# Performance work log

Measured on AMD Instinct MI355X. Metric: run time of the kernel, lower is better.

## Reference

```python
import jax, jax.numpy as jnp
import numpy as np

DIN = 512      # input feature dim (din)
HEADS = 8
DHEAD = 64
DIM = HEADS * DHEAD  # 512
NTOT = 12288   # total nodes across all graphs
NBATCH = 32    # number of graphs
NMAX = 512     # padded max nodes per graph (<= pf_threshold ~562 -> softmax branch)
EPS = 1e-5


def setup_inputs() -> dict:
    key = jax.random.key(0)
    ks = jax.random.split(key, 7)
    z = jax.random.normal(ks[0], (NTOT, DIN), jnp.float32)
    src = jnp.sort(jax.random.randint(ks[1], (NTOT,), 0, NBATCH)).astype(jnp.int32)
    w_scale = 1.0 / np.sqrt(DIN)
    Wq = jax.random.normal(ks[2], (DIN, DIM), jnp.float32) * w_scale
    Wk = jax.random.normal(ks[3], (DIN, DIM), jnp.float32) * w_scale
    Wv = jax.random.normal(ks[4], (DIN, DIM), jnp.float32) * w_scale
    Wo = jax.random.normal(ks[5], (DIM, DIM), jnp.float32) * w_scale
    bo = jnp.zeros((DIM,), jnp.float32)
    ln_gamma = jnp.ones((DIN,), jnp.float32)
    ln_beta = jnp.zeros((DIN,), jnp.float32)
    return {"z": z, "src": src, "ln_gamma": ln_gamma, "ln_beta": ln_beta,
            "Wq": Wq, "Wk": Wk, "Wv": Wv, "Wo": Wo, "bo": bo,
            "n_max": NMAX, "n_batch": NBATCH}


def reference(z, src, ln_gamma, ln_beta, Wq, Wk, Wv, Wo, bo, n_max, n_batch):
    # --- LayerNorm(din) ---
    mu = jnp.mean(z, axis=-1, keepdims=True)
    var = jnp.mean(jnp.square(z - mu), axis=-1, keepdims=True)
    zn = (z - mu) * jax.lax.rsqrt(var + EPS) * ln_gamma + ln_beta

    # --- to_dense_batch(zn, src): src is sorted graph-id per node ---
    ntot = z.shape[0]
    counts = jnp.bincount(src, length=n_batch)                    # [B]
    starts = jnp.concatenate([jnp.zeros((1,), counts.dtype), jnp.cumsum(counts)[:-1]])
    pos = jnp.arange(ntot) - starts[src]                          # position within graph
    x = jnp.zeros((n_batch, n_max, DIN), zn.dtype).at[src, pos].set(zn)   # [B,N,din]
    mask = jnp.zeros((n_batch, n_max), bool).at[src, pos].set(True)       # [B,N]

    # --- q/k/v projections, split heads: b n (h d) -> b h n d ---
    def heads(t):
        return t.reshape(n_batch, n_max, HEADS, DHEAD).transpose(0, 2, 1, 3)
    q = heads(x @ Wq)
    k = heads(x @ Wk)
    v = heads(x @ Wv)

    # --- manual masked softmax attention (N <= pf_threshold branch) ---
    s = jnp.einsum('bhmd,bhnd->bhmn', q, k)
    s = jnp.where(mask[:, None, None, :], s, -jnp.inf)
    a = jax.nn.softmax(s * (DHEAD ** -0.5), axis=-1)
    o = jnp.einsum('bhmn,bhnd->bhmd', a, v)

    # --- merge heads, gather valid rows (out[mask]), output projection ---
    o = o.transpose(0, 2, 1, 3).reshape(n_batch, n_max, DIM)
    h = o[src, pos] @ Wo + bo                                     # [Ntot, DIM]
    return h
```

## Files before the change

kernel.cpp:

```cpp
#include <hip/hip_runtime.h>
#include <hip/hip_bf16.h>
#include <math.h>

#define DIN 512
#define DIM 512
#define NHEADS 8
#define DHEAD 64
#define NB 32
#define NPAD 512
#define NPTOT (NB * NPAD)

typedef __attribute__((ext_vector_type(8))) short bf16x8;
typedef __attribute__((ext_vector_type(8))) unsigned short u16x8;
typedef __attribute__((ext_vector_type(4))) float f32x4;

typedef __attribute__((address_space(3))) unsigned int lds_u32;
typedef __attribute__((address_space(1))) const unsigned int g_u32;

__device__ __forceinline__ void gll16(const unsigned short* g, unsigned short* l) {
  __builtin_amdgcn_global_load_lds((g_u32*)g, (lds_u32*)l, 16, 0, 0);
}

__device__ inline unsigned short f2bf(float x) {
  unsigned int u = __float_as_uint(x);
  unsigned int r = (u + 0x7FFFu + ((u >> 16) & 1u)) >> 16;
  return (unsigned short)r;
}

__global__ __launch_bounds__(256) void prep_kernel(const float* __restrict__ z,
                                                   const float* __restrict__ gamma,
                                                   const float* __restrict__ beta,
                                                   const int* __restrict__ src,
                                                   const float* __restrict__ Wq,
                                                   const float* __restrict__ Wk,
                                                   const float* __restrict__ Wv,
                                                   const float* __restrict__ Wo,
                                                   unsigned short* __restrict__ zn,
                                                   int* __restrict__ starts,
                                                   int* __restrict__ dstrow,
                                                   unsigned short* __restrict__ WtQKV,
                                                   unsigned short* __restrict__ WtO,
                                                   int ntot) {
  __shared__ float tile[32][33];
  int b = blockIdx.x;
  int nln = ntot >> 2;
  int nmap = (ntot + 255) >> 8;
  if (b < nln) {
    int wave = b * 4 + (threadIdx.x >> 6);
    int lane = threadIdx.x & 63;
    const float* row = z + (size_t)wave * DIN;
    float4 a = ((const float4*)row)[lane];
    float4 bb = ((const float4*)row)[64 + lane];
    float s  = a.x + a.y + a.z + a.w + bb.x + bb.y + bb.z + bb.w;
    float sq = a.x*a.x + a.y*a.y + a.z*a.z + a.w*a.w
             + bb.x*bb.x + bb.y*bb.y + bb.z*bb.z + bb.w*bb.w;
#pragma unroll
    for (int off = 32; off; off >>= 1) {
      s  += __shfl_xor(s, off);
      sq += __shfl_xor(sq, off);
    }
    float mu  = s * (1.0f / DIN);
    float var = sq * (1.0f / DIN) - mu * mu;
    float r   = rsqrtf(var + 1e-5f);
    float4 g0 = ((const float4*)gamma)[lane];
    float4 g1 = ((const float4*)gamma)[64 + lane];
    float4 b0 = ((const float4*)beta)[lane];
    float4 b1 = ((const float4*)beta)[64 + lane];
    ushort4 o0, o1;
    o0.x = f2bf((a.x - mu) * r * g0.x + b0.x);
    o0.y = f2bf((a.y - mu) * r * g0.y + b0.y);
    o0.z = f2bf((a.z - mu) * r * g0.z + b0.z);
    o0.w = f2bf((a.w - mu) * r * g0.w + b0.w);
    o1.x = f2bf((bb.x - mu) * r * g1.x + b1.x);
    o1.y = f2bf((bb.y - mu) * r * g1.y + b1.y);
    o1.z = f2bf((bb.z - mu) * r * g1.z + b1.z);
    o1.w = f2bf((bb.w - mu) * r * g1.w + b1.w);
    ((ushort4*)(zn + (size_t)wave * DIN))[lane] = o0;
    ((ushort4*)(zn + (size_t)wave * DIN))[64 + lane] = o1;
  } else if (b < nln + nmap) {
    int bid = b - nln;
    if (bid == 0 && threadIdx.x <= NB) {
      int gg = threadIdx.x;
      int lo = 0, hi = ntot;
      while (lo < hi) { int mid = (lo + hi) >> 1; if (src[mid] < gg) lo = mid + 1; else hi = mid; }
      starts[gg] = lo;
    }
    int i = bid * 256 + threadIdx.x;
    if (i < ntot) {
      int gg = src[i];
      int lo = 0, hi = ntot;
      while (lo < hi) { int mid = (lo + hi) >> 1; if (src[mid] < gg) lo = mid + 1; else hi = mid; }
      dstrow[i] = gg * NPAD + (i - lo);
    }
  } else {
    int idx = b - nln - nmap;
    int zz = idx >> 8;
    int rem = idx & 255;
    const float* W; unsigned short* Wt;
    if (zz == 0)      { W = Wq; Wt = WtQKV; }
    else if (zz == 1) { W = Wk; Wt = WtQKV + (size_t)512 * DIN; }
    else if (zz == 2) { W = Wv; Wt = WtQKV + (size_t)1024 * DIN; }
    else              { W = Wo; Wt = WtO; }
    int k0 = (rem & 15) * 32;
    int n0 = (rem >> 4) * 32;
    int tx = threadIdx.x & 31;
    int ty = threadIdx.x >> 5;
#pragma unroll
    for (int i = 0; i < 4; i++)
      tile[ty + i * 8][tx] = W[(size_t)(k0 + ty + i * 8) * DIM + n0 + tx];
    __syncthreads();
#pragma unroll
    for (int i = 0; i < 4; i++)
      Wt[(size_t)(n0 + ty + i * 8) * DIN + k0 + tx] = f2bf(tile[tx][ty + i * 8]);
  }
}

template <int NCOLS, bool BIAS, bool OUT_F32, bool REMAP>
__global__ __launch_bounds__(256) void gemm_staged(const unsigned short* __restrict__ A,
                                                   const unsigned short* __restrict__ Bt,
                                                   const float* __restrict__ bias,
                                                   const int* __restrict__ remap,
                                                   unsigned short* __restrict__ Cbf,
                                                   float* __restrict__ Cf) {
  __shared__ unsigned short smem[16384];
  int tid = threadIdx.x, lane = tid & 63, wv = tid >> 6;
  int col = lane & 15, quad = lane >> 4;
  int m0 = blockIdx.x * 128, n0 = blockIdx.y * 128;
  int msub = (wv & 1) * 64, nsub = (wv >> 1) * 64;

  int srow = lane >> 2;
  int cswz = (((lane & 3) ^ ((lane >> 3) & 3))) * 8;

  f32x4 acc[4][4];
#pragma unroll
  for (int i = 0; i < 4; i++)
#pragma unroll
    for (int j = 0; j < 4; j++) acc[i][j] = (f32x4){0.f, 0.f, 0.f, 0.f};

  auto stage = [&](int ks, int nb) {
    const unsigned short* Ab = A  + (size_t)m0 * DIN + ks * 32;
    const unsigned short* Bb = Bt + (size_t)n0 * DIN + ks * 32;
#pragma unroll
    for (int i = 0; i < 2; i++) {
      int t = wv * 2 + i;
      gll16(Ab + (size_t)(t * 16 + srow) * DIN + cswz, smem + nb * 4096 + t * 512);
      gll16(Bb + (size_t)(t * 16 + srow) * DIN + cswz, smem + 8192 + nb * 4096 + t * 512);
    }
  };

  stage(0, 0);
#pragma unroll 2
  for (int ks = 0; ks < 16; ks++) {
    int cur = ks & 1;
    __syncthreads();
    if (ks + 1 < 16) stage(ks + 1, 1 - cur);
    bf16x8 af[4], bfr[4];
#pragma unroll
    for (int mt = 0; mt < 4; mt++) {
      int row = msub + mt * 16 + col;
      af[mt] = *(const bf16x8*)&smem[cur * 4096 + row * 32 + ((quad ^ ((row >> 1) & 3)) * 8)];
    }
#pragma unroll
    for (int nt = 0; nt < 4; nt++) {
      int row = nsub + nt * 16 + col;
      bfr[nt] = *(const bf16x8*)&smem[8192 + cur * 4096 + row * 32 + ((quad ^ ((row >> 1) & 3)) * 8)];
    }
#pragma unroll
    for (int mt = 0; mt < 4; mt++)
#pragma unroll
      for (int nt = 0; nt < 4; nt++)
        acc[mt][nt] = __builtin_amdgcn_mfma_f32_16x16x32_bf16(af[mt], bfr[nt], acc[mt][nt], 0, 0, 0);
  }

  if (!OUT_F32) {
    __syncthreads();
#pragma unroll
    for (int mt = 0; mt < 4; mt++)
#pragma unroll
      for (int r = 0; r < 4; r++) {
        int row = msub + mt * 16 + quad * 4 + r;
#pragma unroll
        for (int nt = 0; nt < 4; nt++) {
          int c = nsub + nt * 16 + col;
          float v = acc[mt][nt][r] + (BIAS ? bias[n0 + c] : 0.f);
          smem[row * 128 + (((c >> 3) ^ (quad << 1)) * 8) + (c & 7)] = f2bf(v);
        }
      }
    __syncthreads();
#pragma unroll
    for (int pass = 0; pass < 8; pass++) {
      int row = pass * 16 + (tid >> 4);
      int sw  = ((row >> 2) & 3) << 1;
      int ch  = tid & 15;
      u16x8 vv = *(const u16x8*)&smem[row * 128 + ((ch ^ sw) * 8)];
      int drow = REMAP ? remap[m0 + row] : (m0 + row);
      *(u16x8*)(Cbf + (size_t)drow * NCOLS + n0 + ch * 8) = vv;
    }
  } else {
#pragma unroll
    for (int mt = 0; mt < 4; mt++) {
#pragma unroll
      for (int r = 0; r < 4; r++) {
        int mrow = m0 + msub + mt * 16 + quad * 4 + r;
#pragma unroll
        for (int nt = 0; nt < 4; nt++) {
          int ncol = n0 + nsub + nt * 16 + col;
          Cf[(size_t)mrow * NCOLS + ncol] = acc[mt][nt][r] + (BIAS ? bias[ncol] : 0.f);
        }
      }
    }
  }
}

__global__ __launch_bounds__(256, 3) void fattn_kernel(const unsigned short* __restrict__ qkvp,
                                                       const int* __restrict__ starts,
                                                       unsigned short* __restrict__ obuf) {
  __shared__ unsigned short Kbuf[2][64 * 64];
  __shared__ unsigned short Vbuf[2][64 * 64];
  __shared__ unsigned short Plds[4][32 * 64];
  int g = blockIdx.x, h = blockIdx.y, qt = blockIdx.z;
  int st = starts[g];
  int n  = starts[g + 1] - st;
  int q0b = qt * 128;
  if (q0b >= n) return;
  int tid = threadIdx.x, lane = tid & 63, wv = tid >> 6;
  int col = lane & 15, quad = lane >> 4;
  int q0 = q0b + wv * 32;
  bool active = q0 < n;
  int ntiles = (n + 63) >> 6;

  bf16x8 qf[2][2];
  if (active) {
#pragma unroll
    for (int a = 0; a < 2; a++) {
      const unsigned short* qp = qkvp + (size_t)(g * NPAD + q0 + a * 16 + col) * 1536 + h * 64 + quad * 8;
      qf[a][0] = *(const bf16x8*)(qp);
      qf[a][1] = *(const bf16x8*)(qp + 32);
    }
  }

  int srow = tid >> 2;
  int sc   = (tid & 3) * 2;
  int woff0 = srow * 64 + ((sc ^ (srow & 7)) * 8);
  int woff1 = srow * 64 + (((sc + 1) ^ (srow & 7)) * 8);
  u16x8 kreg0, kreg1, vreg0, vreg1;
  auto loadregs = [&](int kt) {
    const unsigned short* kp = qkvp + (size_t)(g * NPAD + kt + srow) * 1536 + 512 + h * 64 + sc * 8;
    kreg0 = *(const u16x8*)(kp);
    kreg1 = *(const u16x8*)(kp + 8);
    vreg0 = *(const u16x8*)(kp + 512);
    vreg1 = *(const u16x8*)(kp + 520);
  };
  auto writelds = [&](int bsel) {
    *(u16x8*)&Kbuf[bsel][woff0] = kreg0;
    *(u16x8*)&Kbuf[bsel][woff1] = kreg1;
#pragma unroll
    for (int i = 0; i < 8; i++) {
      int c0 = sc * 8 + i;
      int c1 = sc * 8 + 8 + i;
      Vbuf[bsel][c0 * 64 + (((srow >> 3) ^ ((c0 >> 4) << 1) ^ (c0 & 7)) * 8) + (srow & 7)] = vreg0[i];
      Vbuf[bsel][c1 * 64 + (((srow >> 3) ^ ((c1 >> 4) << 1) ^ (c1 & 7)) * 8) + (srow & 7)] = vreg1[i];
    }
  };

  bf16x8 onesv;
#pragma unroll
  for (int i = 0; i < 8; i++) onesv[i] = (short)0x3F80;

  f32x4 oa[2][4];
  f32x4 lacc[2];
#pragma unroll
  for (int a = 0; a < 2; a++) {
    lacc[a] = (f32x4){0.f, 0.f, 0.f, 0.f};
#pragma unroll
    for (int i = 0; i < 4; i++) oa[a][i] = (f32x4){0.f, 0.f, 0.f, 0.f};
  }

  loadregs(0);
  writelds(0);
  __syncthreads();

  for (int t = 0; t < ntiles; t++) {
    int cur = t & 1;
    if (t + 1 < ntiles) loadregs((t + 1) * 64);
    if (active) {
      f32x4 s[2][4];
#pragma unroll
      for (int a = 0; a < 2; a++)
#pragma unroll
        for (int j = 0; j < 4; j++) s[a][j] = (f32x4){0.f, 0.f, 0.f, 0.f};
#pragma unroll
      for (int j = 0; j < 4; j++) {
        int R = j * 16 + col;
        bf16x8 kf0 = *(const bf16x8*)&Kbuf[cur][R * 64 + ((quad ^ (R & 7)) * 8)];
        bf16x8 kf1 = *(const bf16x8*)&Kbuf[cur][R * 64 + (((4 + quad) ^ (R & 7)) * 8)];
        s[0][j] = __builtin_amdgcn_mfma_f32_16x16x32_bf16(qf[0][0], kf0, s[0][j], 0, 0, 0);
        s[0][j] = __builtin_amdgcn_mfma_f32_16x16x32_bf16(qf[0][1], kf1, s[0][j], 0, 0, 0);
        s[1][j] = __builtin_amdgcn_mfma_f32_16x16x32_bf16(qf[1][0], kf0, s[1][j], 0, 0, 0);
        s[1][j] = __builtin_amdgcn_mfma_f32_16x16x32_bf16(qf[1][1], kf1, s[1][j], 0, 0, 0);
      }
      int kt = t * 64;
#pragma unroll
      for (int j = 0; j < 4; j++) {
        bool valid = (kt + j * 16 + col) < n;
#pragma unroll
        for (int a = 0; a < 2; a++)
#pragma unroll
          for (int r = 0; r < 4; r++)
            s[a][j][r] = valid ? __expf(s[a][j][r] * 0.125f) : 0.f;
      }
#pragma unroll
      for (int a = 0; a < 2; a++)
#pragma unroll
        for (int r = 0; r < 4; r++) {
          int R = a * 16 + quad * 4 + r;
#pragma unroll
          for (int j = 0; j < 4; j++) {
            int chunk = j * 2 + (col >> 3);
            Plds[wv][R * 64 + ((chunk ^ (R & 7)) * 8) + (col & 7)] = f2bf(s[a][j][r]);
          }
        }
      __builtin_amdgcn_fence(__ATOMIC_ACQ_REL, "workgroup");
      bf16x8 pf[2][2];
#pragma unroll
      for (int a = 0; a < 2; a++) {
        int R = a * 16 + col;
        pf[a][0] = *(const bf16x8*)&Plds[wv][R * 64 + ((quad ^ (col & 7)) * 8)];
        pf[a][1] = *(const bf16x8*)&Plds[wv][R * 64 + (((4 + quad) ^ (col & 7)) * 8)];
      }
#pragma unroll
      for (int dt = 0; dt < 4; dt++) {
        int R = dt * 16 + col;
        int gR = ((R >> 4) << 1) ^ (R & 7);
        bf16x8 vf0 = *(const bf16x8*)&Vbuf[cur][R * 64 + ((quad ^ gR) * 8)];
        bf16x8 vf1 = *(const bf16x8*)&Vbuf[cur][R * 64 + (((quad + 4) ^ gR) * 8)];
        oa[0][dt] = __builtin_amdgcn_mfma_f32_16x16x32_bf16(pf[0][0], vf0, oa[0][dt], 0, 0, 0);
        oa[0][dt] = __builtin_amdgcn_mfma_f32_16x16x32_bf16(pf[0][1], vf1, oa[0][dt], 0, 0, 0);
        oa[1][dt] = __builtin_amdgcn_mfma_f32_16x16x32_bf16(pf[1][0], vf0, oa[1][dt], 0, 0, 0);
        oa[1][dt] = __builtin_amdgcn_mfma_f32_16x16x32_bf16(pf[1][1], vf1, oa[1][dt], 0, 0, 0);
      }
      lacc[0] = __builtin_amdgcn_mfma_f32_16x16x32_bf16(pf[0][0], onesv, lacc[0], 0, 0, 0);
      lacc[0] = __builtin_amdgcn_mfma_f32_16x16x32_bf16(pf[0][1], onesv, lacc[0], 0, 0, 0);
      lacc[1] = __builtin_amdgcn_mfma_f32_16x16x32_bf16(pf[1][0], onesv, lacc[1], 0, 0, 0);
      lacc[1] = __builtin_amdgcn_mfma_f32_16x16x32_bf16(pf[1][1], onesv, lacc[1], 0, 0, 0);
    }
    if (t + 1 < ntiles) writelds(1 - cur);
    __syncthreads();
  }

  if (active) {
#pragma unroll
    for (int a = 0; a < 2; a++)
#pragma unroll
      for (int r = 0; r < 4; r++) {
        int q = q0 + a * 16 + quad * 4 + r;
        if (q < n) {
          float inv = 1.0f / lacc[a][r];
          unsigned short* op = obuf + (size_t)(st + q) * DIM + h * 64 + col;
          op[0]  = f2bf(oa[a][0][r] * inv);
          op[16] = f2bf(oa[a][1][r] * inv);
          op[32] = f2bf(oa[a][2][r] * inv);
          op[48] = f2bf(oa[a][3][r] * inv);
        }
      }
  }
}

extern "C" void kernel_launch(void* const* d_in, const int* in_sizes, int n_in,
                              void* d_out, int out_size, void* d_ws, size_t ws_size,
                              hipStream_t stream) {
  const float* z     = (const float*)d_in[0];
  const int*   src   = (const int*)d_in[1];
  const float* gamma = (const float*)d_in[2];
  const float* beta  = (const float*)d_in[3];
  const float* Wq    = (const float*)d_in[4];
  const float* Wk    = (const float*)d_in[5];
  const float* Wv    = (const float*)d_in[6];
  const float* Wo    = (const float*)d_in[7];
  const float* bo    = (const float*)d_in[8];
  int ntot = in_sizes[0] / DIN;
  float* out = (float*)d_out;

  char* ws = (char*)d_ws;
  size_t off = 0;
  unsigned short* zn    = (unsigned short*)(ws + off); off += (size_t)ntot * DIN * 2;
  unsigned short* qkvp  = (unsigned short*)(ws + off); off += (size_t)NPTOT * 1536 * 2;
  unsigned short* obuf  = (unsigned short*)(ws + off); off += (size_t)ntot * DIM * 2;
  unsigned short* WtQKV = (unsigned short*)(ws + off); off += (size_t)1536 * DIN * 2;
  unsigned short* WtO   = (unsigned short*)(ws + off); off += (size_t)DIM * DIN * 2;
  int* starts           = (int*)(ws + off);            off += 64 * 4;
  int* dstrow           = (int*)(ws + off);

  int nln = ntot >> 2;
  int nmap = (ntot + 255) >> 8;
  prep_kernel<<<nln + nmap + 1024, 256, 0, stream>>>(z, gamma, beta, src, Wq, Wk, Wv, Wo,
                                                     zn, starts, dstrow, WtQKV, WtO, ntot);

  gemm_staged<1536, false, false, true>
      <<<dim3(ntot / 128, 12), 256, 0, stream>>>(zn, WtQKV, nullptr, dstrow, qkvp, nullptr);

  fattn_kernel<<<dim3(NB, NHEADS, 4), 256, 0, stream>>>(qkvp, starts, obuf);

  gemm_staged<512, true, true, false>
      <<<dim3(ntot / 128, 4), 256, 0, stream>>>(obuf, WtO, bo, nullptr, nullptr, out);
}
```

Baseline: 171.1 us.

## Stage fp32 GEMM output through LDS and pack V transpose writes

The fp32 output path of the GEMM now stages accumulators in swizzled shared memory, half the tile at a time, and then writes coalesced 16-byte vectors to global memory. Before, it issued scattered scalar stores. In the attention kernel, each thread now loads V from two adjacent key rows and writes packed 32-bit pairs into the transposed V buffer, with a new swizzle. This replaces sixteen 16-bit shared-memory stores per thread with eight 32-bit stores. The cost is extra barriers in the GEMM epilogue and a changed LDS swizzle that must stay consistent with the reads.

```diff
diff --git a/kernel.cpp b/kernel.cpp
--- a/kernel.cpp
+++ b/kernel.cpp
@@ -197,15 +197,37 @@
       *(u16x8*)(Cbf + (size_t)drow * NCOLS + n0 + ch * 8) = vv;
     }
   } else {
-#pragma unroll
-    for (int mt = 0; mt < 4; mt++) {
-#pragma unroll
-      for (int r = 0; r < 4; r++) {
-        int mrow = m0 + msub + mt * 16 + quad * 4 + r;
-#pragma unroll
-        for (int nt = 0; nt < 4; nt++) {
-          int ncol = n0 + nsub + nt * 16 + col;
-          Cf[(size_t)mrow * NCOLS + ncol] = acc[mt][nt][r] + (BIAS ? bias[ncol] : 0.f);
+    float* smemf = (float*)smem;
+    float bv[4];
+#pragma unroll
+    for (int nt = 0; nt < 4; nt++) bv[nt] = BIAS ? bias[n0 + nsub + nt * 16 + col] : 0.f;
+#pragma unroll
+    for (int hh = 0; hh < 2; hh++) {
+      __syncthreads();
+      if ((wv & 1) == hh) {
+#pragma unroll
+        for (int mt = 0; mt < 4; mt++)
+#pragma unroll
+          for (int r = 0; r < 4; r++) {
+            int row64 = mt * 16 + quad * 4 + r;
+#pragma unroll
+            for (int nt = 0; nt < 4; nt++) {
+              int c = nsub + nt * 16 + col;
+              smemf[row64 * 128 + (c ^ (quad * 16))] = acc[mt][nt][r] + bv[nt];
+            }
+          }
+      }
+      __syncthreads();
+#pragma unroll
+      for (int p = 0; p < 2; p++) {
+        int row64 = p * 32 + (tid >> 3);
+        int sub = tid & 7;
+        int sw = ((row64 >> 2) & 3) * 16;
+#pragma unroll
+        for (int i = 0; i < 4; i++) {
+          int c = sub * 4 + i * 32;
+          f32x4 v4 = *(const f32x4*)&smemf[row64 * 128 + (c ^ sw)];
+          *(f32x4*)&Cf[(size_t)(m0 + hh * 64 + row64) * NCOLS + n0 + c] = v4;
         }
       }
     }
@@ -241,25 +263,30 @@
 
   int srow = tid >> 2;
   int sc   = (tid & 3) * 2;
-  int woff0 = srow * 64 + ((sc ^ (srow & 7)) * 8);
-  int woff1 = srow * 64 + (((sc + 1) ^ (srow & 7)) * 8);
+  int kwoff0 = srow * 64 + ((sc ^ (srow & 7)) * 8);
+  int kwoff1 = srow * 64 + (((sc + 1) ^ (srow & 7)) * 8);
+  int vkp = tid >> 3;
+  int vdc = tid & 7;
+  int vkc   = vkp >> 2;
+  int vkoff = (vkp & 3) * 2;
   u16x8 kreg0, kreg1, vreg0, vreg1;
   auto loadregs = [&](int kt) {
     const unsigned short* kp = qkvp + (size_t)(g * NPAD + kt + srow) * 1536 + 512 + h * 64 + sc * 8;
     kreg0 = *(const u16x8*)(kp);
     kreg1 = *(const u16x8*)(kp + 8);
-    vreg0 = *(const u16x8*)(kp + 512);
-    vreg1 = *(const u16x8*)(kp + 520);
+    const unsigned short* vp = qkvp + (size_t)(g * NPAD + kt + 2 * vkp) * 1536 + 1024 + h * 64 + vdc * 8;
+    vreg0 = *(const u16x8*)(vp);
+    vreg1 = *(const u16x8*)(vp + 1536);
   };
   auto writelds = [&](int bsel) {
-    *(u16x8*)&Kbuf[bsel][woff0] = kreg0;
-    *(u16x8*)&Kbuf[bsel][woff1] = kreg1;
+    *(u16x8*)&Kbuf[bsel][kwoff0] = kreg0;
+    *(u16x8*)&Kbuf[bsel][kwoff1] = kreg1;
 #pragma unroll
     for (int i = 0; i < 8; i++) {
-      int c0 = sc * 8 + i;
-      int c1 = sc * 8 + 8 + i;
-      Vbuf[bsel][c0 * 64 + (((srow >> 3) ^ ((c0 >> 4) << 1) ^ (c0 & 7)) * 8) + (srow & 7)] = vreg0[i];
-      Vbuf[bsel][c1 * 64 + (((srow >> 3) ^ ((c1 >> 4) << 1) ^ (c1 & 7)) * 8) + (srow & 7)] = vreg1[i];
+      int d = vdc * 8 + i;
+      unsigned int pv = (unsigned int)(unsigned short)vreg0[i]
+                      | ((unsigned int)(unsigned short)vreg1[i] << 16);
+      *(unsigned int*)&Vbuf[bsel][d * 64 + ((vkc ^ (d & 7) ^ (d >> 3)) * 8) + vkoff] = pv;
     }
   };
 
@@ -331,9 +358,9 @@
 #pragma unroll
       for (int dt = 0; dt < 4; dt++) {
         int R = dt * 16 + col;
-        int gR = ((R >> 4) << 1) ^ (R & 7);
-        bf16x8 vf0 = *(const bf16x8*)&Vbuf[cur][R * 64 + ((quad ^ gR) * 8)];
-        bf16x8 vf1 = *(const bf16x8*)&Vbuf[cur][R * 64 + (((quad + 4) ^ gR) * 8)];
+        int swz = (R & 7) ^ (R >> 3);
+        bf16x8 vf0 = *(const bf16x8*)&Vbuf[cur][R * 64 + ((quad ^ swz) * 8)];
+        bf16x8 vf1 = *(const bf16x8*)&Vbuf[cur][R * 64 + (((quad + 4) ^ swz) * 8)];
         oa[0][dt] = __builtin_amdgcn_mfma_f32_16x16x32_bf16(pf[0][0], vf0, oa[0][dt], 0, 0, 0);
         oa[0][dt] = __builtin_amdgcn_mfma_f32_16x16x32_bf16(pf[0][1], vf1, oa[0][dt], 0, 0, 0);
         oa[1][dt] = __builtin_amdgcn_mfma_f32_16x16x32_bf16(pf[1][0], vf0, oa[1][dt], 0, 0, 0);
```

Result: no change. 173.0 us (+1.1%).
